# Kernel optimization log

Hardware: AMD Instinct MI355X
Metric: run time of the kernel (lower is better)

Reference implementation:

```python
import jax, jax.numpy as jnp
import numpy as np
from jax import lax


def conv3x3(x, w):
    # x: (B,C,H,W), w: (O,I,3,3); stride 1, padding 1, no bias
    return lax.conv_general_dilated(x, w, (1, 1), 'SAME',
                                    dimension_numbers=('NCHW', 'OIHW', 'NCHW'))


def group_norm(x, w, b, groups=32, eps=1e-5):
    B, C, H, W = x.shape
    xg = x.reshape(B, groups, C // groups, H, W)
    mu = xg.mean(axis=(2, 3, 4), keepdims=True)
    var = xg.var(axis=(2, 3, 4), keepdims=True)
    xg = (xg - mu) * lax.rsqrt(var + eps)
    return xg.reshape(B, C, H, W) * w[None, :, None, None] + b[None, :, None, None]


def to_patches(x, p1, p2):
    # 'b c (h p1) (w p2) -> (b h w) c (p1 p2)'
    B, C, H, W = x.shape
    h, w = H // p1, W // p2
    x = x.reshape(B, C, h, p1, w, p2).transpose(0, 2, 4, 1, 3, 5)
    return x.reshape(B * h * w, C, p1 * p2)


def from_patches(x, B, h, w, p1, p2):
    # '(b h w) c (p1 p2) -> b c (h p1) (w p2)'
    C = x.shape[1]
    x = x.reshape(B, h, w, C, p1, p2).transpose(0, 3, 1, 4, 2, 5)
    return x.reshape(B, C, h * p1, w * p2)


def setup_inputs() -> dict:
    key = jax.random.key(0)
    ks = jax.random.split(key, 5)
    B, C, H, W = 8, 256, 128, 128
    inter = 256
    s = 0.05  # keep conv outputs in a sane range
    return {
        'x_low': jax.random.normal(ks[0], (B, C, H, W), jnp.float32),
        'x_high': jax.random.normal(ks[1], (B, C, H, W), jnp.float32),
        'w_q': jax.random.normal(ks[2], (inter, C, 3, 3), jnp.float32) * s,
        'gq_w': jnp.ones((inter,), jnp.float32),
        'gq_b': jnp.zeros((inter,), jnp.float32),
        'w_k': jax.random.normal(ks[3], (inter, C, 3, 3), jnp.float32) * s,
        'gk_w': jnp.ones((inter,), jnp.float32),
        'gk_b': jnp.zeros((inter,), jnp.float32),
        'w_o': jax.random.normal(ks[4], (C, inter, 3, 3), jnp.float32) * s,
        'go_w': jnp.ones((C,), jnp.float32),
        'go_b': jnp.zeros((C,), jnp.float32),
        'p1': 8,
        'p2': 8,
    }


def reference(x_low, x_high, w_q, gq_w, gq_b, w_k, gk_w, gk_b, w_o, go_w, go_b, p1, p2):
    B, C, H, W = x_low.shape
    inter = w_q.shape[0]
    h, w = H // p1, W // p2
    # q, k: (B*h*w, inter, T) with T = p1*p2
    q = to_patches(group_norm(conv3x3(x_low, w_q), gq_w, gq_b), p1, p2)
    k = to_patches(group_norm(conv3x3(x_high, w_k), gk_w, gk_b), p1, p2)
    q = q.transpose(0, 2, 1)                                  # (N, T, inter)
    attn = jnp.matmul(q, k) / jnp.sqrt(jnp.float32(inter))    # (N, T, T)
    attn = jax.nn.softmax(attn, axis=-1)
    out = jnp.matmul(attn, k.transpose(0, 2, 1))              # (N, T, inter)
    out = from_patches(out.transpose(0, 2, 1), B, h, w, p1, p2)
    return group_norm(conv3x3(out + x_low, w_o), go_w, go_b)
```

## Files before the change

### kernel.cpp

```cpp
#include <hip/hip_runtime.h>

using u16 = unsigned short;
using u32 = unsigned int;

typedef short bfrag8 __attribute__((ext_vector_type(8)));
typedef float f32x4  __attribute__((ext_vector_type(4)));

__device__ __forceinline__ void unpack8(const int4 v, float f[8]) {
  u32 a = (u32)v.x, b = (u32)v.y, c = (u32)v.z, d = (u32)v.w;
  f[0] = __uint_as_float(a << 16);
  f[1] = __uint_as_float(a & 0xffff0000u);
  f[2] = __uint_as_float(b << 16);
  f[3] = __uint_as_float(b & 0xffff0000u);
  f[4] = __uint_as_float(c << 16);
  f[5] = __uint_as_float(c & 0xffff0000u);
  f[6] = __uint_as_float(d << 16);
  f[7] = __uint_as_float(d & 0xffff0000u);
}

__device__ __forceinline__ u16 f2bf(float f) {
  u32 u = __float_as_uint(f);
  u32 r = u + 0x7fffu + ((u >> 16) & 1u);
  return (u16)(r >> 16);
}

__device__ __forceinline__ void gload_lds16(const void* g, void* l) {
  __builtin_amdgcn_global_load_lds(
      (const __attribute__((address_space(1))) void*)g,
      (__attribute__((address_space(3))) void*)l, 16, 0, 0);
}

__global__ __launch_bounds__(256) void wprep(
    const float* __restrict__ wq, const float* __restrict__ wk, const float* __restrict__ wo,
    u16* __restrict__ dq, u16* __restrict__ dk, u16* __restrict__ dwo)
{
  const float* s = (blockIdx.y == 0) ? wq : (blockIdx.y == 1) ? wk : wo;
  u16* d = (blockIdx.y == 0) ? dq : (blockIdx.y == 1) ? dk : dwo;
  int id = blockIdx.x * 256 + threadIdx.x;
  int e = id * 4;
  int tap = e >> 16;
  int rem = e & 65535;
  int oc = rem >> 8, ic = rem & 255;
  u16 o[4];
#pragma unroll
  for (int j = 0; j < 4; ++j)
    o[j] = f2bf(s[((size_t)oc * 256 + ic + j) * 9 + tap]);
  *reinterpret_cast<uint2*>(d + e) = *reinterpret_cast<uint2*>(o);
}

__global__ __launch_bounds__(256) void xpose(
    const float* __restrict__ xa, const float* __restrict__ xb,
    u16* __restrict__ oa, u16* __restrict__ ob)
{
  const int row = blockIdx.x, b = blockIdx.y;
  const float* src = blockIdx.z ? xb : xa;
  u16* dst = blockIdx.z ? ob : oa;
  const int t = threadIdx.x;
  const int px4 = (t >> 3) * 4;
  const int c8 = (t & 7) * 8;
#pragma unroll
  for (int p = 0; p < 4; ++p) {
    int c0 = p * 64 + c8;
    float4 v[8];
#pragma unroll
    for (int j = 0; j < 8; ++j)
      v[j] = *reinterpret_cast<const float4*>(src + ((size_t)b * 256 + c0 + j) * 16384 + row * 128 + px4);
#pragma unroll
    for (int e = 0; e < 4; ++e) {
      u16 o[8];
      o[0] = f2bf(e==0?v[0].x:e==1?v[0].y:e==2?v[0].z:v[0].w);
      o[1] = f2bf(e==0?v[1].x:e==1?v[1].y:e==2?v[1].z:v[1].w);
      o[2] = f2bf(e==0?v[2].x:e==1?v[2].y:e==2?v[2].z:v[2].w);
      o[3] = f2bf(e==0?v[3].x:e==1?v[3].y:e==2?v[3].z:v[3].w);
      o[4] = f2bf(e==0?v[4].x:e==1?v[4].y:e==2?v[4].z:v[4].w);
      o[5] = f2bf(e==0?v[5].x:e==1?v[5].y:e==2?v[5].z:v[5].w);
      o[6] = f2bf(e==0?v[6].x:e==1?v[6].y:e==2?v[6].z:v[6].w);
      o[7] = f2bf(e==0?v[7].x:e==1?v[7].y:e==2?v[7].z:v[7].w);
      *reinterpret_cast<int4*>(dst + (((size_t)b * 128 + row) * 128 + px4 + e) * 256 + c0) =
          *reinterpret_cast<int4*>(o);
    }
  }
}

__global__ __launch_bounds__(512, 4) void conv_mfma(
    const u16* __restrict__ X, const u16* __restrict__ W2, u16* __restrict__ Y,
    float* __restrict__ part)
{
  __shared__ __attribute__((aligned(16))) char csm[74496];

  const int t = threadIdx.x;
  const int l = t & 63;
  const int wv = t >> 6;
  const int id = blockIdx.x;
  const int u = (id & 7) * 128 + (id >> 3);
  const int bb = u >> 7, y0 = u & 127;
  const int och = wv >> 1, pxh = wv & 1;
  const int lc = l & 15, lq = l >> 4;
  const int sa = (lc >> 1) & 3;

  f32x4 acc[4][4];
#pragma unroll
  for (int m = 0; m < 4; ++m)
#pragma unroll
    for (int n = 0; n < 4; ++n) acc[m][n] = (f32x4){0.f, 0.f, 0.f, 0.f};

  const size_t xplane = (size_t)bb * (128 * 128 * 256);

  {
    int4 z = {0, 0, 0, 0};
    if (t < 24) {
      int q = t & 3, sel = (t >> 2) & 1, kh = t >> 3;
      int cidx = sel ? 129 : 0;
      *reinterpret_cast<int4*>(csm + ((kh * 132 + cidx) * 4 + q) * 16) = z;
    }
    if (y0 == 0)
      for (int s = t; s < 528; s += 512) *reinterpret_cast<int4*>(csm + s * 16) = z;
    if (y0 == 127)
      for (int s = t; s < 528; s += 512) *reinterpret_cast<int4*>(csm + 16896 + s * 16) = z;
  }

  auto stageA = [&](int tap, int buf, int ic0) {
#pragma unroll
    for (int i = 0; i < 2; ++i) {
      int idx = t + i * 512;
      int oc = idx >> 2, q = idx & 3;
      int qs = q ^ ((oc >> 1) & 3);
      const u16* src = W2 + (((size_t)(tap * 256 + oc)) << 8) + ic0 + qs * 8;
      gload_lds16(src, csm + 25344 + buf * 16384 + (i * 512 + (t & ~63)) * 16);
    }
  };
  auto stageB = [&](int ic0) {
#pragma unroll
    for (int i = 0; i < 3; ++i) {
      int idx = t + i * 512;
      int kh = idx >> 9;
      int row = y0 - 1 + kh;
      if (row >= 0 && row < 128) {
        int px = (idx & 511) >> 2, q = idx & 3;
        int qs = q ^ (((px + 1) >> 1) & 3);
        const u16* src = X + xplane + (((size_t)(row * 128 + px)) << 8) + ic0 + qs * 8;
        gload_lds16(src, csm + 64 + kh * 256 + (i * 512 + (t & ~63)) * 16);
      }
    }
  };

  stageB(0);
  stageA(0, 0, 0);
  stageA(1, 1, 0);
  __syncthreads();

  for (int chunk = 0; chunk < 8; ++chunk) {
    const int ic0 = chunk * 32;
#pragma unroll
    for (int tap = 0; tap < 9; ++tap) {
      const int kh = tap / 3, kw = tap % 3, buf = tap % 3;
      if (tap <= 6) stageA(tap + 2, (tap + 2) % 3, ic0);

      bfrag8 af[4], xf[4];
      const int sb = ((lc + kw) >> 1) & 3;
#pragma unroll
      for (int m = 0; m < 4; ++m)
        af[m] = *reinterpret_cast<const bfrag8*>(csm + 25344 + buf * 16384 +
                    (((och * 64 + m * 16 + lc) * 4) + (lq ^ sa)) * 16);
#pragma unroll
      for (int n = 0; n < 4; ++n) {
        int S = pxh * 64 + n * 16 + lc + kw;
        xf[n] = *reinterpret_cast<const bfrag8*>(csm + kh * 8448 + S * 64 + (lq ^ sb) * 16);
      }
      asm volatile("s_waitcnt lgkmcnt(0)" ::: "memory");
      __builtin_amdgcn_sched_barrier(0);
      if (tap <= 6) {
        asm volatile("s_waitcnt vmcnt(2)" ::: "memory");
      } else if (tap == 7) {
        asm volatile("s_waitcnt vmcnt(0)" ::: "memory");
      }
      __builtin_amdgcn_sched_barrier(0);
      __builtin_amdgcn_s_barrier();
      __builtin_amdgcn_sched_barrier(0);

      __builtin_amdgcn_s_setprio(1);
#pragma unroll
      for (int m = 0; m < 4; ++m)
#pragma unroll
        for (int n = 0; n < 4; ++n)
          acc[m][n] = __builtin_amdgcn_mfma_f32_16x16x32_bf16(af[m], xf[n], acc[m][n], 0, 0, 0);
      __builtin_amdgcn_s_setprio(0);
    }
    if (chunk < 7) {
      stageA(0, 0, ic0 + 32);
      stageA(1, 1, ic0 + 32);
      stageB(ic0 + 32);
      __syncthreads();
    }
  }

  u16* Ost = (u16*)csm;
  float* sst = (float*)(csm + 67584);
  const int chb = och * 64 + lq * 4;
  const int pxb = pxh * 64 + lc;
#pragma unroll
  for (int m = 0; m < 4; ++m)
#pragma unroll
    for (int n = 0; n < 4; ++n) {
      u32 lo = (u32)f2bf(acc[m][n][0]) | ((u32)f2bf(acc[m][n][1]) << 16);
      u32 hi = (u32)f2bf(acc[m][n][2]) | ((u32)f2bf(acc[m][n][3]) << 16);
      uint2 pk = {lo, hi};
      *reinterpret_cast<uint2*>(&Ost[(pxb + n * 16) * 264 + chb + m * 16]) = pk;
    }
#pragma unroll
  for (int m = 0; m < 4; ++m)
#pragma unroll
    for (int r = 0; r < 4; ++r) {
      float s  = acc[m][0][r] + acc[m][1][r] + acc[m][2][r] + acc[m][3][r];
      float ss = acc[m][0][r] * acc[m][0][r] + acc[m][1][r] * acc[m][1][r] +
                 acc[m][2][r] * acc[m][2][r] + acc[m][3][r] * acc[m][3][r];
#pragma unroll
      for (int off = 1; off < 16; off <<= 1) {
        s  += __shfl_xor(s, off);
        ss += __shfl_xor(ss, off);
      }
      if (lc == 0) {
        int c = och * 64 + m * 16 + lq * 4 + r;
        sst[pxh * 512 + c]       = s;
        sst[pxh * 512 + 256 + c] = ss;
      }
    }
  __syncthreads();

  if (t < 256) {
    float s  = sst[t]       + sst[512 + t];
    float ss = sst[256 + t] + sst[768 + t];
    size_t pb = (((size_t)bb * 128 + y0) * 256 + t) * 2;
    part[pb]     = s;
    part[pb + 1] = ss;
  }
#pragma unroll
  for (int s8 = 0; s8 < 8; ++s8) {
    int pix = s8 * 16 + (t >> 5);
    int sub = t & 31;
    int4 v = *reinterpret_cast<const int4*>(&Ost[pix * 264 + sub * 8]);
    *reinterpret_cast<int4*>(Y + xplane + (((size_t)(y0 * 128 + pix)) << 8) + sub * 8) = v;
  }
}

__global__ __launch_bounds__(256) void gnstat2b(const float* __restrict__ part, float* __restrict__ stat)
{
  const int b = blockIdx.x, t = threadIdx.x;
  float s = 0.f, ss = 0.f;
  for (int row = 0; row < 128; ++row) {
    size_t pb = (((size_t)b * 128 + row) * 256 + t) * 2;
    s  += part[pb];
    ss += part[pb + 1];
  }
  __shared__ float Ls[256], Lss[256];
  Ls[t] = s; Lss[t] = ss;
  __syncthreads();
  if (t < 32) {
    float S = 0.f, SS = 0.f;
#pragma unroll
    for (int j = 0; j < 8; ++j) { S += Ls[t * 8 + j]; SS += Lss[t * 8 + j]; }
    float mean = S * (1.f / 131072.f);
    float var = SS * (1.f / 131072.f) - mean * mean;
    stat[b * 32 + t] = mean;
    stat[256 + b * 32 + t] = rsqrtf(var + 1e-5f);
  }
}

__global__ __launch_bounds__(256) void normkT(
    const u16* __restrict__ yk, const float* __restrict__ statk,
    const float* __restrict__ gkw, const float* __restrict__ gkb,
    u16* __restrict__ kT)
{
  __shared__ u16 L[8][264];
  const int y = blockIdx.x, b = blockIdx.y;
  const int ph = y >> 3, py = y & 7;
  const int t = threadIdx.x;
  const int px = t >> 5, c8 = (t & 31) * 8;
  const int g = c8 >> 3;
  float mean = statk[b * 32 + g], rstd = statk[256 + b * 32 + g];
  float A[8], Bv[8];
#pragma unroll
  for (int j = 0; j < 8; ++j) {
    A[j] = rstd * gkw[c8 + j];
    Bv[j] = gkb[c8 + j] - mean * A[j];
  }
  const size_t rowbase = (((size_t)b * 128 + y) * 128) * 256;
  const size_t outbase = ((size_t)(b * 16 + ph) * 8 + py) * 32768;
  for (int pw = 0; pw < 16; ++pw) {
    int4 v = *reinterpret_cast<const int4*>(yk + rowbase + (size_t)(pw * 8 + px) * 256 + c8);
    float f[8]; unpack8(v, f);
    u16 o[8];
#pragma unroll
    for (int j = 0; j < 8; ++j) o[j] = f2bf(f[j] * A[j] + Bv[j]);
    *reinterpret_cast<int4*>(&L[px][c8]) = *reinterpret_cast<int4*>(o);
    __syncthreads();
    u16 o2[8];
#pragma unroll
    for (int q = 0; q < 8; ++q) o2[q] = L[q][t];
    *reinterpret_cast<int4*>(kT + outbase + (size_t)(pw * 256 + t) * 8) = *reinterpret_cast<int4*>(o2);
    __syncthreads();
  }
}

#define OST 280
__global__ __launch_bounds__(256, 3) void attn_mfma(
    const u16* __restrict__ yq, const u16* __restrict__ yk,
    const u16* __restrict__ kT, const u16* __restrict__ xl,
    const float* __restrict__ statq, const float* __restrict__ statk,
    const float* __restrict__ gqw, const float* __restrict__ gqb,
    const float* __restrict__ gkw,
    u16* __restrict__ resid)
{
  __shared__ __attribute__((aligned(16))) u16 smem[64 * OST + 4 * 16 * 72];
  u16* Ost = smem;
  u16* Pls = smem + 64 * OST;

  const int n = blockIdx.x;
  const int b = n >> 8, ph = (n >> 4) & 15, pw = n & 15;
  const int t = threadIdx.x, l = t & 63, w = t >> 6;
  const int lc = l & 15, lg = l >> 4;

  auto tokaddr = [&](int tok) -> size_t {
    return (((size_t)(b * 128 + ph * 8 + (tok >> 3))) * 128 + pw * 8 + (tok & 7)) * 256;
  };

  const size_t qa = tokaddr(16 * w + lc) + lg * 8;
  bfrag8 aF[8];
#pragma unroll
  for (int ks = 0; ks < 8; ++ks) {
    int c0 = lg * 8 + ks * 32;
    int g = ks * 4 + lg;
    float meanq = statq[b * 32 + g], rstdq = statq[256 + b * 32 + g];
    float rstdk = statk[256 + b * 32 + g];
    int4 v = *reinterpret_cast<const int4*>(yq + qa + ks * 32);
    float f[8]; unpack8(v, f);
    float4 w0 = *reinterpret_cast<const float4*>(gqw + c0);
    float4 w1 = *reinterpret_cast<const float4*>(gqw + c0 + 4);
    float4 b0 = *reinterpret_cast<const float4*>(gqb + c0);
    float4 b1 = *reinterpret_cast<const float4*>(gqb + c0 + 4);
    float4 k0 = *reinterpret_cast<const float4*>(gkw + c0);
    float4 k1 = *reinterpret_cast<const float4*>(gkw + c0 + 4);
    float ww[8] = {w0.x, w0.y, w0.z, w0.w, w1.x, w1.y, w1.z, w1.w};
    float bb[8] = {b0.x, b0.y, b0.z, b0.w, b1.x, b1.y, b1.z, b1.w};
    float kk[8] = {k0.x, k0.y, k0.z, k0.w, k1.x, k1.y, k1.z, k1.w};
    u16 o[8];
#pragma unroll
    for (int j = 0; j < 8; ++j) {
      float Aq = rstdq * ww[j];
      float Bq = bb[j] - meanq * Aq;
      float Ak = rstdk * kk[j];
      o[j] = f2bf((f[j] * Aq + Bq) * Ak);
    }
    aF[ks] = *reinterpret_cast<bfrag8*>(o);
  }

  f32x4 sacc[4];
#pragma unroll
  for (int nt = 0; nt < 4; ++nt) sacc[nt] = (f32x4){0.f, 0.f, 0.f, 0.f};

#pragma unroll
  for (int nt = 0; nt < 4; ++nt) {
    const size_t ka = tokaddr(nt * 16 + lc) + lg * 8;
    bfrag8 bF[8];
#pragma unroll
    for (int ks = 0; ks < 8; ++ks)
      bF[ks] = *reinterpret_cast<const bfrag8*>(yk + ka + ks * 32);
#pragma unroll
    for (int ks = 0; ks < 8; ++ks)
      sacc[nt] = __builtin_amdgcn_mfma_f32_16x16x32_bf16(aF[ks], bF[ks], sacc[nt], 0, 0, 0);
  }

  u16* Pw = Pls + w * (16 * 72);
#pragma unroll
  for (int r = 0; r < 4; ++r) {
    float m0 = fmaxf(fmaxf(sacc[0][r], sacc[1][r]), fmaxf(sacc[2][r], sacc[3][r]));
    m0 = fmaxf(m0, __shfl_xor(m0, 1));
    m0 = fmaxf(m0, __shfl_xor(m0, 2));
    m0 = fmaxf(m0, __shfl_xor(m0, 4));
    m0 = fmaxf(m0, __shfl_xor(m0, 8));
    float p0 = __expf((sacc[0][r] - m0) * 0.0625f);
    float p1 = __expf((sacc[1][r] - m0) * 0.0625f);
    float p2 = __expf((sacc[2][r] - m0) * 0.0625f);
    float p3 = __expf((sacc[3][r] - m0) * 0.0625f);
    float s0 = p0 + p1 + p2 + p3;
    s0 += __shfl_xor(s0, 1);
    s0 += __shfl_xor(s0, 2);
    s0 += __shfl_xor(s0, 4);
    s0 += __shfl_xor(s0, 8);
    float inv = 1.f / s0;
    int prow = (lg * 4 + r) * 72;
    Pw[prow + 0 * 16 + lc] = f2bf(p0 * inv);
    Pw[prow + 1 * 16 + lc] = f2bf(p1 * inv);
    Pw[prow + 2 * 16 + lc] = f2bf(p2 * inv);
    Pw[prow + 3 * 16 + lc] = f2bf(p3 * inv);
  }

  bfrag8 pA[2];
#pragma unroll
  for (int js = 0; js < 2; ++js)
    pA[js] = *reinterpret_cast<const bfrag8*>(Pw + lc * 72 + js * 32 + lg * 8);

  f32x4 pacc[16];
#pragma unroll
  for (int ct = 0; ct < 16; ++ct) pacc[ct] = (f32x4){0.f, 0.f, 0.f, 0.f};

#pragma unroll
  for (int ct = 0; ct < 16; ++ct) {
    bfrag8 vB[2];
#pragma unroll
    for (int js = 0; js < 2; ++js)
      vB[js] = *reinterpret_cast<const bfrag8*>(
          kT + ((size_t)((b * 16 + ph) * 8 + js * 4 + lg)) * 32768 +
          (size_t)(pw * 256 + ct * 16 + lc) * 8);
#pragma unroll
    for (int js = 0; js < 2; ++js)
      pacc[ct] = __builtin_amdgcn_mfma_f32_16x16x32_bf16(pA[js], vB[js], pacc[ct], 0, 0, 0);
  }

#pragma unroll
  for (int ct = 0; ct < 16; ++ct)
#pragma unroll
    for (int r = 0; r < 4; ++r)
      Ost[(16 * w + lg * 4 + r) * OST + ct * 16 + lc] = f2bf(pacc[ct][r]);
  __syncthreads();

#pragma unroll
  for (int s = 0; s < 8; ++s) {
    int px_ = t >> 5;
    int c16 = t & 31;
    size_t g = (((size_t)b * 128 + ph * 8 + s) * 128 + pw * 8 + px_) * 256 + c16 * 8;
    int4 o = *reinterpret_cast<const int4*>(&Ost[(s * 8 + px_) * OST + c16 * 8]);
    int4 r = *reinterpret_cast<const int4*>(xl + g);
    float fo[8], fr[8]; unpack8(o, fo); unpack8(r, fr);
    u16 pk[8];
#pragma unroll
    for (int j = 0; j < 8; ++j) pk[j] = f2bf(fo[j] + fr[j]);
    *reinterpret_cast<int4*>(resid + g) = *reinterpret_cast<int4*>(pk);
  }
}

__global__ __launch_bounds__(256) void gnapply_t(
    const u16* __restrict__ Y, const float* __restrict__ stat,
    const float* __restrict__ gw, const float* __restrict__ gb,
    float* __restrict__ out)
{
  const int row = blockIdx.x, b = blockIdx.y;
  const int t = threadIdx.x;
  const int px4 = (t & 31) * 4;
  const int c8 = (t >> 5) * 8;
#pragma unroll
  for (int p = 0; p < 4; ++p) {
    int c0 = p * 64 + c8;
    int g = c0 >> 3;
    float mean = stat[b * 32 + g], rstd = stat[256 + b * 32 + g];
    float A[8], Bv[8];
#pragma unroll
    for (int j = 0; j < 8; ++j) {
      A[j] = rstd * gw[c0 + j];
      Bv[j] = gb[c0 + j] - mean * A[j];
    }
    float vals[4][8];
#pragma unroll
    for (int e = 0; e < 4; ++e) {
      int4 v = *reinterpret_cast<const int4*>(Y + (((size_t)b * 128 + row) * 128 + px4 + e) * 256 + c0);
      float f[8]; unpack8(v, f);
#pragma unroll
      for (int j = 0; j < 8; ++j) vals[e][j] = fmaf(f[j], A[j], Bv[j]);
    }
#pragma unroll
    for (int j = 0; j < 8; ++j) {
      float4 o = {vals[0][j], vals[1][j], vals[2][j], vals[3][j]};
      *reinterpret_cast<float4*>(out + ((size_t)b * 256 + c0 + j) * 16384 + row * 128 + px4) = o;
    }
  }
}

extern "C" void kernel_launch(void* const* d_in, const int* in_sizes, int n_in,
                              void* d_out, int out_size, void* d_ws, size_t ws_size,
                              hipStream_t stream)
{
  const float* x_low  = (const float*)d_in[0];
  const float* x_high = (const float*)d_in[1];
  const float* w_q    = (const float*)d_in[2];
  const float* gq_w   = (const float*)d_in[3];
  const float* gq_b   = (const float*)d_in[4];
  const float* w_k    = (const float*)d_in[5];
  const float* gk_w   = (const float*)d_in[6];
  const float* gk_b   = (const float*)d_in[7];
  const float* w_o    = (const float*)d_in[8];
  const float* go_w   = (const float*)d_in[9];
  const float* go_b   = (const float*)d_in[10];
  float* out = (float*)d_out;

  char* ws = (char*)d_ws;
  const size_t slot = 67108864;
  u16* xl  = (u16*)(ws + 0 * slot);
  u16* xh  = (u16*)(ws + 1 * slot);
  u16* yq  = (u16*)(ws + 2 * slot);
  u16* yk  = (u16*)(ws + 3 * slot);
  u16* kT  = (u16*)(ws + 4 * slot);
  u16* W2q = (u16*)(ws + 5 * slot);
  u16* W2k = W2q + 589824;
  u16* W2o = W2k + 589824;
  float* partq = (float*)(ws + 5 * slot + 3 * 1179648);
  float* partk = partq + 524288;
  float* parto = partk + 524288;
  float* statq = parto + 524288;
  float* statk = statq + 512;
  float* stato = statk + 512;

  wprep<<<dim3(576, 3), 256, 0, stream>>>(w_q, w_k, w_o, W2q, W2k, W2o);
  xpose<<<dim3(128, 8, 2), 256, 0, stream>>>(x_low, x_high, xl, xh);
  conv_mfma<<<1024, 512, 0, stream>>>(xl, W2q, yq, partq);
  conv_mfma<<<1024, 512, 0, stream>>>(xh, W2k, yk, partk);
  gnstat2b<<<8, 256, 0, stream>>>(partq, statq);
  gnstat2b<<<8, 256, 0, stream>>>(partk, statk);
  normkT<<<dim3(128, 8), 256, 0, stream>>>(yk, statk, gk_w, gk_b, kT);
  attn_mfma<<<2048, 256, 0, stream>>>(yq, yk, kT, xl, statq, statk,
                                      gq_w, gq_b, gk_w, xh);
  conv_mfma<<<1024, 512, 0, stream>>>(xh, W2o, xl, parto);
  gnstat2b<<<8, 256, 0, stream>>>(parto, stato);
  gnapply_t<<<dim3(128, 8), 256, 0, stream>>>(xl, stato, go_w, go_b, out);
}
```

Measured before the change: 692.3 us.

## Switch conv MFMA to 32x32x16 tiles and prefetch fragments before barrier

The conv kernel's inner product moves from 16x16x32 bf16 MFMAs on a 4x4 tile grid to 32x32x16 MFMAs on a 2x2 grid. Each wave now issues fewer LDS fragment reads and fewer MFMA instructions per tap. The loop is also reordered so the next tap's LDS fragments are read right after the barrier, following the MFMAs of the current tap. The epilogue's bf16 store and group-norm partial-sum reductions are rewritten for the 32x32 accumulator layout, which uses a wider shuffle reduction.

```diff
diff --git a/kernel.cpp b/kernel.cpp
--- a/kernel.cpp
+++ b/kernel.cpp
@@ -5,6 +5,7 @@
 
 typedef short bfrag8 __attribute__((ext_vector_type(8)));
 typedef float f32x4  __attribute__((ext_vector_type(4)));
+typedef float f32x16 __attribute__((ext_vector_type(16)));
 
 __device__ __forceinline__ void unpack8(const int4 v, float f[8]) {
   u32 a = (u32)v.x, b = (u32)v.y, c = (u32)v.z, d = (u32)v.w;
@@ -95,14 +96,16 @@
   const int u = (id & 7) * 128 + (id >> 3);
   const int bb = u >> 7, y0 = u & 127;
   const int och = wv >> 1, pxh = wv & 1;
-  const int lc = l & 15, lq = l >> 4;
-  const int sa = (lc >> 1) & 3;
-
-  f32x4 acc[4][4];
-#pragma unroll
-  for (int m = 0; m < 4; ++m)
-#pragma unroll
-    for (int n = 0; n < 4; ++n) acc[m][n] = (f32x4){0.f, 0.f, 0.f, 0.f};
+  const int l31 = l & 31, hi = l >> 5;
+  const int selA = (l31 >> 1) & 3;
+
+  f32x16 acc[2][2];
+#pragma unroll
+  for (int m = 0; m < 2; ++m)
+#pragma unroll
+    for (int nn = 0; nn < 2; ++nn)
+#pragma unroll
+      for (int r = 0; r < 16; ++r) acc[m][nn][r] = 0.f;
 
   const size_t xplane = (size_t)bb * (128 * 128 * 256);
 
@@ -144,6 +147,26 @@
     }
   };
 
+  bfrag8 af[2][2], xf[2][2];
+  auto read_frags = [&](int tap) {
+    const int kh = tap / 3, kw = tap % 3, buf = tap % 3;
+#pragma unroll
+    for (int m = 0; m < 2; ++m)
+#pragma unroll
+      for (int kk = 0; kk < 2; ++kk)
+        af[m][kk] = *reinterpret_cast<const bfrag8*>(csm + 25344 + buf * 16384 +
+            (och * 64 + m * 32 + l31) * 64 + ((2 * kk + hi) ^ selA) * 16);
+#pragma unroll
+    for (int nn = 0; nn < 2; ++nn) {
+      int S = pxh * 64 + nn * 32 + l31 + kw;
+      int selB = (S >> 1) & 3;
+#pragma unroll
+      for (int kk = 0; kk < 2; ++kk)
+        xf[nn][kk] = *reinterpret_cast<const bfrag8*>(csm + kh * 8448 + S * 64 +
+            ((2 * kk + hi) ^ selB) * 16);
+    }
+  };
+
   stageB(0);
   stageA(0, 0, 0);
   stageA(1, 1, 0);
@@ -151,40 +174,37 @@
 
   for (int chunk = 0; chunk < 8; ++chunk) {
     const int ic0 = chunk * 32;
+    read_frags(0);
+    asm volatile("s_waitcnt lgkmcnt(0)" ::: "memory");
+    __builtin_amdgcn_sched_barrier(0);
 #pragma unroll
     for (int tap = 0; tap < 9; ++tap) {
-      const int kh = tap / 3, kw = tap % 3, buf = tap % 3;
-      if (tap <= 6) stageA(tap + 2, (tap + 2) % 3, ic0);
-
-      bfrag8 af[4], xf[4];
-      const int sb = ((lc + kw) >> 1) & 3;
-#pragma unroll
-      for (int m = 0; m < 4; ++m)
-        af[m] = *reinterpret_cast<const bfrag8*>(csm + 25344 + buf * 16384 +
-                    (((och * 64 + m * 16 + lc) * 4) + (lq ^ sa)) * 16);
-#pragma unroll
-      for (int n = 0; n < 4; ++n) {
-        int S = pxh * 64 + n * 16 + lc + kw;
-        xf[n] = *reinterpret_cast<const bfrag8*>(csm + kh * 8448 + S * 64 + (lq ^ sb) * 16);
+      if (tap < 7) stageA(tap + 2, (tap + 2) % 3, ic0);
+
+      __builtin_amdgcn_s_setprio(1);
+#pragma unroll
+      for (int kk = 0; kk < 2; ++kk)
+#pragma unroll
+        for (int m = 0; m < 2; ++m)
+#pragma unroll
+          for (int nn = 0; nn < 2; ++nn)
+            acc[m][nn] = __builtin_amdgcn_mfma_f32_32x32x16_bf16(
+                af[m][kk], xf[nn][kk], acc[m][nn], 0, 0, 0);
+      __builtin_amdgcn_s_setprio(0);
+
+      if (tap < 8) {
+        if (tap < 7) {
+          asm volatile("s_waitcnt vmcnt(2)" ::: "memory");
+        } else {
+          asm volatile("s_waitcnt vmcnt(0)" ::: "memory");
+        }
+        __builtin_amdgcn_sched_barrier(0);
+        __builtin_amdgcn_s_barrier();
+        __builtin_amdgcn_sched_barrier(0);
+        read_frags(tap + 1);
+        asm volatile("s_waitcnt lgkmcnt(0)" ::: "memory");
+        __builtin_amdgcn_sched_barrier(0);
       }
-      asm volatile("s_waitcnt lgkmcnt(0)" ::: "memory");
-      __builtin_amdgcn_sched_barrier(0);
-      if (tap <= 6) {
-        asm volatile("s_waitcnt vmcnt(2)" ::: "memory");
-      } else if (tap == 7) {
-        asm volatile("s_waitcnt vmcnt(0)" ::: "memory");
-      }
-      __builtin_amdgcn_sched_barrier(0);
-      __builtin_amdgcn_s_barrier();
-      __builtin_amdgcn_sched_barrier(0);
-
-      __builtin_amdgcn_s_setprio(1);
-#pragma unroll
-      for (int m = 0; m < 4; ++m)
-#pragma unroll
-        for (int n = 0; n < 4; ++n)
-          acc[m][n] = __builtin_amdgcn_mfma_f32_16x16x32_bf16(af[m], xf[n], acc[m][n], 0, 0, 0);
-      __builtin_amdgcn_s_setprio(0);
     }
     if (chunk < 7) {
       stageA(0, 0, ic0 + 32);
@@ -196,31 +216,33 @@
 
   u16* Ost = (u16*)csm;
   float* sst = (float*)(csm + 67584);
-  const int chb = och * 64 + lq * 4;
-  const int pxb = pxh * 64 + lc;
-#pragma unroll
-  for (int m = 0; m < 4; ++m)
-#pragma unroll
-    for (int n = 0; n < 4; ++n) {
-      u32 lo = (u32)f2bf(acc[m][n][0]) | ((u32)f2bf(acc[m][n][1]) << 16);
-      u32 hi = (u32)f2bf(acc[m][n][2]) | ((u32)f2bf(acc[m][n][3]) << 16);
-      uint2 pk = {lo, hi};
-      *reinterpret_cast<uint2*>(&Ost[(pxb + n * 16) * 264 + chb + m * 16]) = pk;
-    }
-#pragma unroll
-  for (int m = 0; m < 4; ++m)
-#pragma unroll
-    for (int r = 0; r < 4; ++r) {
-      float s  = acc[m][0][r] + acc[m][1][r] + acc[m][2][r] + acc[m][3][r];
-      float ss = acc[m][0][r] * acc[m][0][r] + acc[m][1][r] * acc[m][1][r] +
-                 acc[m][2][r] * acc[m][2][r] + acc[m][3][r] * acc[m][3][r];
-#pragma unroll
-      for (int off = 1; off < 16; off <<= 1) {
+#pragma unroll
+  for (int m = 0; m < 2; ++m)
+#pragma unroll
+    for (int nn = 0; nn < 2; ++nn) {
+      int px = pxh * 64 + nn * 32 + l31;
+#pragma unroll
+      for (int rg = 0; rg < 4; ++rg) {
+        int oc = och * 64 + m * 32 + 8 * rg + 4 * hi;
+        u16 o[4] = {f2bf(acc[m][nn][rg * 4 + 0]), f2bf(acc[m][nn][rg * 4 + 1]),
+                    f2bf(acc[m][nn][rg * 4 + 2]), f2bf(acc[m][nn][rg * 4 + 3])};
+        *reinterpret_cast<uint2*>(&Ost[px * 264 + oc]) = *reinterpret_cast<uint2*>(o);
+      }
+    }
+#pragma unroll
+  for (int m = 0; m < 2; ++m)
+#pragma unroll
+    for (int rg = 0; rg < 16; ++rg) {
+      float a0 = acc[m][0][rg], a1 = acc[m][1][rg];
+      float s  = a0 + a1;
+      float ss = a0 * a0 + a1 * a1;
+#pragma unroll
+      for (int off = 1; off < 32; off <<= 1) {
         s  += __shfl_xor(s, off);
         ss += __shfl_xor(ss, off);
       }
-      if (lc == 0) {
-        int c = och * 64 + m * 16 + lq * 4 + r;
+      if (l31 == 0) {
+        int c = och * 64 + m * 32 + (rg & 3) + 8 * (rg >> 2) + 4 * hi;
         sst[pxh * 512 + c]       = s;
         sst[pxh * 512 + 256 + c] = ss;
       }
```

New measurement: 782.3 us. +13.0%, slower.

## Split conv blocks by output-channel half and double-buffer LDS fragment reads

Applied to the files above, without the earlier changes.

Each conv block now computes 128 output channels instead of 256, using 256 threads with a smaller LDS footprint and twice as many blocks. This aims for more resident blocks per CU. The tap loop now prefetches the next tap's A/B fragments from LDS into alternate register sets while the current tap's MFMAs run, to hide LDS latency. In exchange, each input row tile is loaded twice (once per channel half), which raises global traffic, and the extra fragment registers may limit occupancy.

```diff
diff --git a/kernel.cpp b/kernel.cpp
--- a/kernel.cpp
+++ b/kernel.cpp
@@ -82,18 +82,21 @@
   }
 }
 
-__global__ __launch_bounds__(512, 4) void conv_mfma(
+__global__ __launch_bounds__(256, 3) void conv_mfma(
     const u16* __restrict__ X, const u16* __restrict__ W2, u16* __restrict__ Y,
     float* __restrict__ part)
 {
-  __shared__ __attribute__((aligned(16))) char csm[74496];
+  __shared__ __attribute__((aligned(16))) char csm[49920];
 
   const int t = threadIdx.x;
   const int l = t & 63;
   const int wv = t >> 6;
   const int id = blockIdx.x;
-  const int u = (id & 7) * 128 + (id >> 3);
-  const int bb = u >> 7, y0 = u & 127;
+  const int u = (id & 7) * 256 + (id >> 3);
+  const int bb = u >> 8;
+  const int y0 = (u >> 1) & 127;
+  const int ocblk = u & 1;
+  const int oc0 = ocblk * 128;
   const int och = wv >> 1, pxh = wv & 1;
   const int lc = l & 15, lq = l >> 4;
   const int sa = (lc >> 1) & 3;
@@ -114,35 +117,63 @@
       *reinterpret_cast<int4*>(csm + ((kh * 132 + cidx) * 4 + q) * 16) = z;
     }
     if (y0 == 0)
-      for (int s = t; s < 528; s += 512) *reinterpret_cast<int4*>(csm + s * 16) = z;
+      for (int s = t; s < 528; s += 256) *reinterpret_cast<int4*>(csm + s * 16) = z;
     if (y0 == 127)
-      for (int s = t; s < 528; s += 512) *reinterpret_cast<int4*>(csm + 16896 + s * 16) = z;
+      for (int s = t; s < 528; s += 256) *reinterpret_cast<int4*>(csm + 16896 + s * 16) = z;
   }
 
   auto stageA = [&](int tap, int buf, int ic0) {
 #pragma unroll
     for (int i = 0; i < 2; ++i) {
-      int idx = t + i * 512;
+      int idx = t + i * 256;
       int oc = idx >> 2, q = idx & 3;
       int qs = q ^ ((oc >> 1) & 3);
-      const u16* src = W2 + (((size_t)(tap * 256 + oc)) << 8) + ic0 + qs * 8;
-      gload_lds16(src, csm + 25344 + buf * 16384 + (i * 512 + (t & ~63)) * 16);
+      const u16* src = W2 + (((size_t)(tap * 256 + oc0 + oc)) << 8) + ic0 + qs * 8;
+      gload_lds16(src, csm + 25344 + buf * 8192 + (i * 256 + (t & ~63)) * 16);
     }
   };
   auto stageB = [&](int ic0) {
 #pragma unroll
-    for (int i = 0; i < 3; ++i) {
-      int idx = t + i * 512;
+    for (int i = 0; i < 6; ++i) {
+      int idx = t + i * 256;
       int kh = idx >> 9;
       int row = y0 - 1 + kh;
       if (row >= 0 && row < 128) {
         int px = (idx & 511) >> 2, q = idx & 3;
         int qs = q ^ (((px + 1) >> 1) & 3);
         const u16* src = X + xplane + (((size_t)(row * 128 + px)) << 8) + ic0 + qs * 8;
-        gload_lds16(src, csm + 64 + kh * 256 + (i * 512 + (t & ~63)) * 16);
+        gload_lds16(src, csm + 64 + kh * 256 + (i * 256 + (t & ~63)) * 16);
       }
     }
   };
+
+  bfrag8 af0[4], xf0[4], af1[4], xf1[4];
+
+#define READF(TAP, AF, XF)                                                    \
+  {                                                                           \
+    const int kh_ = (TAP) / 3, kw_ = (TAP) % 3, buf_ = (TAP) % 3;             \
+    const int sb_ = ((lc + kw_) >> 1) & 3;                                    \
+    _Pragma("unroll")                                                         \
+    for (int m = 0; m < 4; ++m)                                               \
+      AF[m] = *reinterpret_cast<const bfrag8*>(csm + 25344 + buf_ * 8192 +    \
+                  ((och * 64 + m * 16 + lc) * 4 + (lq ^ sa)) * 16);           \
+    _Pragma("unroll")                                                         \
+    for (int n = 0; n < 4; ++n) {                                             \
+      int S_ = pxh * 64 + n * 16 + lc + kw_;                                  \
+      XF[n] = *reinterpret_cast<const bfrag8*>(csm + kh_ * 8448 + S_ * 64 +   \
+                  (lq ^ sb_) * 16);                                           \
+    }                                                                         \
+  }
+
+#define DOMFMA(AF, XF)                                                        \
+  {                                                                           \
+    _Pragma("unroll")                                                         \
+    for (int m = 0; m < 4; ++m)                                               \
+      _Pragma("unroll")                                                       \
+      for (int n = 0; n < 4; ++n)                                             \
+        acc[m][n] = __builtin_amdgcn_mfma_f32_16x16x32_bf16(AF[m], XF[n],     \
+                                                            acc[m][n], 0, 0, 0); \
+  }
 
   stageB(0);
   stageA(0, 0, 0);
@@ -151,24 +182,12 @@
 
   for (int chunk = 0; chunk < 8; ++chunk) {
     const int ic0 = chunk * 32;
+    READF(0, af0, xf0);
 #pragma unroll
     for (int tap = 0; tap < 9; ++tap) {
-      const int kh = tap / 3, kw = tap % 3, buf = tap % 3;
-      if (tap <= 6) stageA(tap + 2, (tap + 2) % 3, ic0);
-
-      bfrag8 af[4], xf[4];
-      const int sb = ((lc + kw) >> 1) & 3;
-#pragma unroll
-      for (int m = 0; m < 4; ++m)
-        af[m] = *reinterpret_cast<const bfrag8*>(csm + 25344 + buf * 16384 +
-                    (((och * 64 + m * 16 + lc) * 4) + (lq ^ sa)) * 16);
-#pragma unroll
-      for (int n = 0; n < 4; ++n) {
-        int S = pxh * 64 + n * 16 + lc + kw;
-        xf[n] = *reinterpret_cast<const bfrag8*>(csm + kh * 8448 + S * 64 + (lq ^ sb) * 16);
-      }
       asm volatile("s_waitcnt lgkmcnt(0)" ::: "memory");
       __builtin_amdgcn_sched_barrier(0);
+      if (tap <= 6) stageA(tap + 2, (tap + 2) % 3, ic0);
       if (tap <= 6) {
         asm volatile("s_waitcnt vmcnt(2)" ::: "memory");
       } else if (tap == 7) {
@@ -178,12 +197,13 @@
       __builtin_amdgcn_s_barrier();
       __builtin_amdgcn_sched_barrier(0);
 
+      if (tap < 8) {
+        if (tap & 1) { READF(tap + 1, af0, xf0); }
+        else         { READF(tap + 1, af1, xf1); }
+      }
       __builtin_amdgcn_s_setprio(1);
-#pragma unroll
-      for (int m = 0; m < 4; ++m)
-#pragma unroll
-        for (int n = 0; n < 4; ++n)
-          acc[m][n] = __builtin_amdgcn_mfma_f32_16x16x32_bf16(af[m], xf[n], acc[m][n], 0, 0, 0);
+      if (tap & 1) { DOMFMA(af1, xf1); }
+      else         { DOMFMA(af0, xf0); }
       __builtin_amdgcn_s_setprio(0);
     }
     if (chunk < 7) {
@@ -193,11 +213,14 @@
       __syncthreads();
     }
   }
+#undef READF
+#undef DOMFMA
 
   u16* Ost = (u16*)csm;
-  float* sst = (float*)(csm + 67584);
+  float* sst = (float*)(csm + 34816);
   const int chb = och * 64 + lq * 4;
   const int pxb = pxh * 64 + lc;
+  __syncthreads();
 #pragma unroll
   for (int m = 0; m < 4; ++m)
 #pragma unroll
@@ -205,7 +228,7 @@
       u32 lo = (u32)f2bf(acc[m][n][0]) | ((u32)f2bf(acc[m][n][1]) << 16);
       u32 hi = (u32)f2bf(acc[m][n][2]) | ((u32)f2bf(acc[m][n][3]) << 16);
       uint2 pk = {lo, hi};
-      *reinterpret_cast<uint2*>(&Ost[(pxb + n * 16) * 264 + chb + m * 16]) = pk;
+      *reinterpret_cast<uint2*>(&Ost[(pxb + n * 16) * 136 + chb + m * 16]) = pk;
     }
 #pragma unroll
   for (int m = 0; m < 4; ++m)
@@ -221,25 +244,25 @@
       }
       if (lc == 0) {
         int c = och * 64 + m * 16 + lq * 4 + r;
-        sst[pxh * 512 + c]       = s;
-        sst[pxh * 512 + 256 + c] = ss;
+        sst[pxh * 256 + c]       = s;
+        sst[pxh * 256 + 128 + c] = ss;
       }
     }
   __syncthreads();
 
-  if (t < 256) {
-    float s  = sst[t]       + sst[512 + t];
-    float ss = sst[256 + t] + sst[768 + t];
-    size_t pb = (((size_t)bb * 128 + y0) * 256 + t) * 2;
+  if (t < 128) {
+    float s  = sst[t]       + sst[256 + t];
+    float ss = sst[128 + t] + sst[384 + t];
+    size_t pb = (((size_t)bb * 128 + y0) * 256 + oc0 + t) * 2;
     part[pb]     = s;
     part[pb + 1] = ss;
   }
 #pragma unroll
   for (int s8 = 0; s8 < 8; ++s8) {
-    int pix = s8 * 16 + (t >> 5);
-    int sub = t & 31;
-    int4 v = *reinterpret_cast<const int4*>(&Ost[pix * 264 + sub * 8]);
-    *reinterpret_cast<int4*>(Y + xplane + (((size_t)(y0 * 128 + pix)) << 8) + sub * 8) = v;
+    int pix = s8 * 16 + (t >> 4);
+    int sub = t & 15;
+    int4 v = *reinterpret_cast<const int4*>(&Ost[pix * 136 + sub * 8]);
+    *reinterpret_cast<int4*>(Y + xplane + (((size_t)(y0 * 128 + pix)) << 8) + oc0 + sub * 8) = v;
   }
 }
 
@@ -511,14 +534,14 @@
 
   wprep<<<dim3(576, 3), 256, 0, stream>>>(w_q, w_k, w_o, W2q, W2k, W2o);
   xpose<<<dim3(128, 8, 2), 256, 0, stream>>>(x_low, x_high, xl, xh);
-  conv_mfma<<<1024, 512, 0, stream>>>(xl, W2q, yq, partq);
-  conv_mfma<<<1024, 512, 0, stream>>>(xh, W2k, yk, partk);
+  conv_mfma<<<2048, 256, 0, stream>>>(xl, W2q, yq, partq);
+  conv_mfma<<<2048, 256, 0, stream>>>(xh, W2k, yk, partk);
   gnstat2b<<<8, 256, 0, stream>>>(partq, statq);
   gnstat2b<<<8, 256, 0, stream>>>(partk, statk);
   normkT<<<dim3(128, 8), 256, 0, stream>>>(yk, statk, gk_w, gk_b, kT);
   attn_mfma<<<2048, 256, 0, stream>>>(yq, yk, kT, xl, statq, statk,
                                       gq_w, gq_b, gk_w, xh);
-  conv_mfma<<<1024, 512, 0, stream>>>(xh, W2o, xl, parto);
+  conv_mfma<<<2048, 256, 0, stream>>>(xh, W2o, xl, parto);
   gnstat2b<<<8, 256, 0, stream>>>(parto, stato);
   gnapply_t<<<dim3(128, 8), 256, 0, stream>>>(xl, stato, go_w, go_b, out);
 }
```

Measured after the change: 696.3 us. No clear change (+0.6%).
